# Kernel optimization log

Hardware: AMD Instinct MI355X
Metric: run time of the kernel (lower is better)

## Reference

```python
import jax, jax.numpy as jnp
import numpy as np

N = 524288
IN_C = 128
OUT_C = 128
NUM_GRAPHS = 64
NUM_STROKES = 8192
EPS = 1e-5


def setup_inputs() -> dict:
    key = jax.random.key(0)
    ks = jax.random.split(key, 8)
    x = jax.random.normal(ks[0], (N, IN_C), dtype=jnp.float32)
    batch = jnp.sort(jax.random.randint(ks[1], (N,), 0, NUM_GRAPHS))
    stroke_idx = jnp.sort(jax.random.randint(ks[2], (N,), 0, NUM_STROKES))
    s = 1.0 / np.sqrt(IN_C)
    W_max = jax.random.uniform(ks[3], (IN_C, OUT_C), jnp.float32, -s, s)
    b_max = jax.random.uniform(ks[4], (OUT_C,), jnp.float32, -s, s)
    g_max = jnp.ones((OUT_C,), jnp.float32)
    be_max = jnp.zeros((OUT_C,), jnp.float32)
    W_sk = jax.random.uniform(ks[5], (IN_C, OUT_C), jnp.float32, -s, s)
    b_sk = jax.random.uniform(ks[6], (OUT_C,), jnp.float32, -s, s)
    g_sk = jnp.ones((OUT_C,), jnp.float32)
    be_sk = jnp.zeros((OUT_C,), jnp.float32)
    return {"x": x, "batch": batch, "stroke_idx": stroke_idx,
            "W_max": W_max, "b_max": b_max, "g_max": g_max, "be_max": be_max,
            "W_sk": W_sk, "b_sk": b_sk, "g_sk": g_sk, "be_sk": be_sk}


def _mlp(x, W, b, gamma, beta):
    # Linear -> BatchNorm1d (training-mode batch stats, biased var) -> ReLU
    h = x @ W + b
    mu = jnp.mean(h, axis=0)
    var = jnp.mean((h - mu) ** 2, axis=0)
    h = (h - mu) * jax.lax.rsqrt(var + EPS) * gamma + beta
    return jax.nn.relu(h)


def reference(x, batch, stroke_idx, W_max, b_max, g_max, be_max, W_sk, b_sk, g_sk, be_sk):
    pool_max = _mlp(x, W_max, b_max, g_max, be_max)      # (N, F)
    pool_sketch = _mlp(x, W_sk, b_sk, g_sk, be_sk)       # (N, F)
    # segment max-pool per graph / per stroke, then broadcast back to nodes
    gmax = jax.ops.segment_max(pool_max, batch, num_segments=NUM_GRAPHS)       # (G, F)
    smax = jax.ops.segment_max(pool_sketch, stroke_idx, num_segments=NUM_STROKES)  # (S, F)
    pool_max = gmax[batch]          # (N, F)
    pool_sketch = smax[stroke_idx]  # (N, F)
    return jnp.concatenate([pool_sketch, pool_max], axis=1)  # (N, 2F)
```

## Files before the change

### kernel.cpp

```cpp
#include <hip/hip_runtime.h>
#include <hip/hip_bf16.h>
#include <climits>
#include <cstdint>
#include <cfloat>

#define NROWS   524288
#define KDIM    128
#define NGRAPH  64
#define NSTROKE 8192
#define EPSF    1e-5f

typedef __bf16 bf16x8 __attribute__((ext_vector_type(8)));
typedef float  f32x4  __attribute__((ext_vector_type(4)));

#define WT_OFF    0
#define CSUM_OFF  65536
#define CSQ_OFF   66560
#define ST_OFF    67584
#define GT_OFF    (ST_OFF + NSTROKE*KDIM*4)

__device__ __forceinline__ unsigned short f2bf(float f) {
  unsigned int u = __float_as_uint(f);
  u += 0x7fffu + ((u >> 16) & 1u);
  return (unsigned short)(u >> 16);
}
__device__ __forceinline__ int fkey(float f) {
  int b = __float_as_int(f);
  return b >= 0 ? b : (b ^ 0x7fffffff);
}
__device__ __forceinline__ float fdec(int k) {
  int b = k >= 0 ? k : (k ^ 0x7fffffff);
  return __int_as_float(b);
}

__global__ void k_init(const float* __restrict__ Wmax, const float* __restrict__ Wsk,
                       unsigned char* __restrict__ ws) {
  unsigned short* wt = (unsigned short*)(ws + WT_OFF);
  float* csum = (float*)(ws + CSUM_OFF);
  float* csq  = (float*)(ws + CSQ_OFF);
  int* st = (int*)(ws + ST_OFF);
  int* gt = (int*)(ws + GT_OFF);
  int i = blockIdx.x * blockDim.x + threadIdx.x;
  const int total = NSTROKE * KDIM;
  for (; i < total; i += gridDim.x * blockDim.x) {
    st[i] = INT_MIN;
    if (i < NGRAPH * KDIM) gt[i] = INT_MIN;
    if (i < 256) { csum[i] = 0.f; csq[i] = 0.f; }
    if (i < 256 * KDIM) {
      int c = i / KDIM, k = i % KDIM;
      float w = (c < 128) ? Wsk[k * 128 + c] : Wmax[k * 128 + (c - 128)];
      wt[i] = f2bf(w);
    }
  }
}

__global__ __launch_bounds__(256) void k_pass1(const float* __restrict__ x,
                                               const int* __restrict__ batch,
                                               const int* __restrict__ stroke,
                                               unsigned char* __restrict__ ws) {
  __shared__ __align__(16) unsigned short xs[2][64 * 128];
  const unsigned short* wt = (const unsigned short*)(ws + WT_OFF);
  float* csum = (float*)(ws + CSUM_OFF);
  float* csq  = (float*)(ws + CSQ_OFF);
  int* st = (int*)(ws + ST_OFF);
  int* gt = (int*)(ws + GT_OFF);

  const int tid  = threadIdx.x;
  const int lane = tid & 63;
  const int wv   = tid >> 6;
  const int lr   = lane & 15;
  const int lg   = lane >> 4;
  const int srow = tid >> 4;
  const int skg  = tid & 15;

  bf16x8 bfrag[4][4];
#pragma unroll
  for (int ks = 0; ks < 4; ++ks)
#pragma unroll
    for (int n = 0; n < 4; ++n) {
      int c = wv * 64 + n * 16 + lr;
      int k = ks * 32 + lg * 8;
      bfrag[ks][n] = *(const bf16x8*)(wt + c * KDIM + k);
    }

  float sumn[4] = {0.f, 0.f, 0.f, 0.f};
  float sqn[4]  = {0.f, 0.f, 0.f, 0.f};

  const bool isS = (wv < 2);
  const int* __restrict__ segp = isS ? stroke : batch;
  int* __restrict__ tab = isS ? st : gt;
  const int tcol = (isS ? wv : wv - 2) * 64;

  int   curseg = -1;
  float runmax[4] = {-FLT_MAX, -FLT_MAX, -FLT_MAX, -FLT_MAX};

#define FLUSH()                                                               \
  if (curseg >= 0) {                                                          \
    _Pragma("unroll")                                                         \
    for (int n = 0; n < 4; ++n) {                                             \
      float f = runmax[n];                                                    \
      f = fmaxf(f, __shfl_xor(f, 16));                                        \
      f = fmaxf(f, __shfl_xor(f, 32));                                        \
      if (lg == 0) atomicMax(&tab[curseg * KDIM + tcol + n * 16 + lr], fkey(f)); \
    }                                                                         \
  }

#define PF_LOAD(ROW0)                                                         \
  {                                                                           \
    _Pragma("unroll")                                                         \
    for (int it = 0; it < 4; ++it) {                                          \
      const float* src = x + (size_t)((ROW0) + it * 16 + srow) * KDIM + skg * 8; \
      pf[it * 2]     = *(const f32x4*)src;                                    \
      pf[it * 2 + 1] = *(const f32x4*)(src + 4);                              \
    }                                                                         \
  }

#define PF_STORE(P)                                                           \
  {                                                                           \
    _Pragma("unroll")                                                         \
    for (int it = 0; it < 4; ++it) {                                          \
      int r = it * 16 + srow;                                                 \
      union { bf16x8 v; unsigned short u[8]; } pk;                            \
      f32x4 v0 = pf[it * 2], v1 = pf[it * 2 + 1];                             \
      pk.u[0] = f2bf(v0[0]); pk.u[1] = f2bf(v0[1]);                           \
      pk.u[2] = f2bf(v0[2]); pk.u[3] = f2bf(v0[3]);                           \
      pk.u[4] = f2bf(v1[0]); pk.u[5] = f2bf(v1[1]);                           \
      pk.u[6] = f2bf(v1[2]); pk.u[7] = f2bf(v1[3]);                           \
      *(bf16x8*)(xs[P] + r * KDIM + ((skg ^ (r & 7)) << 3)) = pk.v;           \
    }                                                                         \
  }

  const int brow = blockIdx.x * 512;
  f32x4 pf[8];
  int segv, segnext;

  PF_LOAD(brow);
  segv = segp[brow + lane];
  PF_STORE(0);
  __syncthreads();

  int cur = 0;
  for (int ti = 0; ti < 8; ++ti) {
    if (ti < 7) {
      PF_LOAD(brow + (ti + 1) * 64);
      segnext = segp[brow + (ti + 1) * 64 + lane];
    }

    f32x4 acc[4][4];
#pragma unroll
    for (int m = 0; m < 4; ++m)
#pragma unroll
      for (int n = 0; n < 4; ++n) { f32x4 z = {0.f, 0.f, 0.f, 0.f}; acc[m][n] = z; }

#pragma unroll
    for (int ks = 0; ks < 4; ++ks) {
      bf16x8 af[4];
#pragma unroll
      for (int m = 0; m < 4; ++m) {
        int r  = m * 16 + lr;
        int kg = ks * 4 + lg;
        af[m] = *(const bf16x8*)(xs[cur] + r * KDIM + ((kg ^ (r & 7)) << 3));
      }
#pragma unroll
      for (int m = 0; m < 4; ++m)
#pragma unroll
        for (int n = 0; n < 4; ++n)
          acc[m][n] = __builtin_amdgcn_mfma_f32_16x16x32_bf16(af[m], bfrag[ks][n], acc[m][n], 0, 0, 0);
    }

    float tm[4];
#pragma unroll
    for (int n = 0; n < 4; ++n) {
      float s = 0.f, q = 0.f, t = -FLT_MAX;
#pragma unroll
      for (int m = 0; m < 4; ++m)
#pragma unroll
        for (int rg = 0; rg < 4; ++rg) {
          float v = acc[m][n][rg];
          s += v; q = fmaf(v, v, q); t = fmaxf(t, v);
        }
      sumn[n] += s; sqn[n] += q; tm[n] = t;
    }

    {
      int pv = __shfl_up(segv, 1);
      unsigned long long mask = __ballot(lane > 0 && pv != segv);
      if (mask == 0ull) {
        int seg0 = __shfl(segv, 0);
        if (seg0 == curseg) {
#pragma unroll
          for (int n = 0; n < 4; ++n) runmax[n] = fmaxf(runmax[n], tm[n]);
        } else {
          FLUSH();
          curseg = seg0;
#pragma unroll
          for (int n = 0; n < 4; ++n) runmax[n] = tm[n];
        }
      } else {
        unsigned long long rem = mask;
        int a = 0;
        while (true) {
          int b = rem ? (int)__builtin_ctzll(rem) : 64;
          int segr = __shfl(segv, a);
          float rm[4] = {-FLT_MAX, -FLT_MAX, -FLT_MAX, -FLT_MAX};
#pragma unroll
          for (int m = 0; m < 4; ++m)
#pragma unroll
            for (int rg = 0; rg < 4; ++rg) {
              int pos = m * 16 + lg * 4 + rg;
              bool in = (pos >= a) && (pos < b);
#pragma unroll
              for (int n = 0; n < 4; ++n)
                rm[n] = in ? fmaxf(rm[n], acc[m][n][rg]) : rm[n];
            }
          if (a == 0 && segr == curseg) {
#pragma unroll
            for (int n = 0; n < 4; ++n) runmax[n] = fmaxf(runmax[n], rm[n]);
          } else {
            FLUSH();
            curseg = segr;
#pragma unroll
            for (int n = 0; n < 4; ++n) runmax[n] = rm[n];
          }
          if (b >= 64) break;
          rem &= rem - 1; a = b;
        }
      }
    }

    if (ti < 7) {
      PF_STORE(cur ^ 1);
      segv = segnext;
    }
    __syncthreads();
    cur ^= 1;
  }

  FLUSH();

#pragma unroll
  for (int n = 0; n < 4; ++n) {
    sumn[n] += __shfl_xor(sumn[n], 16);
    sumn[n] += __shfl_xor(sumn[n], 32);
    sqn[n]  += __shfl_xor(sqn[n], 16);
    sqn[n]  += __shfl_xor(sqn[n], 32);
  }
  float s = 0.f, q = 0.f;
#pragma unroll
  for (int n = 0; n < 4; ++n) if (n == lg) { s = sumn[n]; q = sqn[n]; }
  atomicAdd(&csum[tid], s);
  atomicAdd(&csq[tid], q);
#undef FLUSH
#undef PF_LOAD
#undef PF_STORE
}

__global__ __launch_bounds__(256) void k_out(const int* __restrict__ batch,
                                             const int* __restrict__ stroke,
                                             const float* __restrict__ g_max,
                                             const float* __restrict__ be_max,
                                             const float* __restrict__ g_sk,
                                             const float* __restrict__ be_sk,
                                             const unsigned char* __restrict__ ws,
                                             float* __restrict__ out) {
  const float* csum = (const float*)(ws + CSUM_OFF);
  const float* csq  = (const float*)(ws + CSQ_OFF);
  const int* st = (const int*)(ws + ST_OFF);
  const int* gt = (const int*)(ws + GT_OFF);

  const int lane = threadIdx.x & 63;
  const int wvid = blockIdx.x * 4 + (threadIdx.x >> 6);
  const int row0 = wvid * 64;
  const bool isS = lane < 32;
  const int  cg  = (isS ? lane : lane - 32) * 4;
  const int* tab  = isS ? st : gt;
  const int* idxp = isS ? stroke : batch;
  const float* gv = isS ? g_sk : g_max;
  const float* bv = isS ? be_sk : be_max;

  const float invN = 1.0f / (float)NROWS;
  f32x4 mu, sc, bb;
#pragma unroll
  for (int j = 0; j < 4; ++j) {
    int cc = (isS ? 0 : 128) + cg + j;
    float m  = csum[cc] * invN;
    float vr = csq[cc] * invN - m * m;
    mu[j] = m;
    sc[j] = gv[cg + j] * rsqrtf(vr + EPSF);
    bb[j] = bv[cg + j];
  }

  f32x4* out4 = (f32x4*)out;
#pragma unroll 4
  for (int r = 0; r < 64; ++r) {
    int row = row0 + r;
    int seg = idxp[row];
    const int4 k4 = *(const int4*)(tab + (size_t)seg * KDIM + cg);
    f32x4 v;
    v[0] = fdec(k4.x); v[1] = fdec(k4.y); v[2] = fdec(k4.z); v[3] = fdec(k4.w);
#pragma unroll
    for (int j = 0; j < 4; ++j) v[j] = fmaxf(0.f, (v[j] - mu[j]) * sc[j] + bb[j]);
    __builtin_nontemporal_store(v, &out4[(size_t)row * 64 + lane]);
  }
}

extern "C" void kernel_launch(void* const* d_in, const int* in_sizes, int n_in,
                              void* d_out, int out_size, void* d_ws, size_t ws_size,
                              hipStream_t stream) {
  const float* x      = (const float*)d_in[0];
  const int*   batch  = (const int*)d_in[1];
  const int*   stroke = (const int*)d_in[2];
  const float* Wmax   = (const float*)d_in[3];
  const float* g_max  = (const float*)d_in[5];
  const float* be_max = (const float*)d_in[6];
  const float* Wsk    = (const float*)d_in[7];
  const float* g_sk   = (const float*)d_in[9];
  const float* be_sk  = (const float*)d_in[10];
  unsigned char* ws = (unsigned char*)d_ws;
  float* out = (float*)d_out;

  k_init <<<2048, 512, 0, stream>>>(Wmax, Wsk, ws);
  k_pass1<<<1024, 256, 0, stream>>>(x, batch, stroke, ws);
  k_out  <<<2048, 256, 0, stream>>>(batch, stroke, g_max, be_max, g_sk, be_sk, ws, out);
}
```

Measured before the change: 244.0 us.

## Split pass1 work across 8 waves with 32 output columns each

The GEMM+segment-max kernel now runs 512 threads per block, with each wave owning 32 output columns instead of 64. This halves per-thread accumulators, B fragments and prefetch registers, which should raise occupancy and hide more latency. In exchange there are more redundant A-fragment LDS reads per tile, plus more segment-boundary scans and atomics, because more waves each handle the same rows.

```diff
diff --git a/kernel.cpp b/kernel.cpp
--- a/kernel.cpp
+++ b/kernel.cpp
@@ -54,10 +54,10 @@
   }
 }
 
-__global__ __launch_bounds__(256) void k_pass1(const float* __restrict__ x,
-                                               const int* __restrict__ batch,
-                                               const int* __restrict__ stroke,
-                                               unsigned char* __restrict__ ws) {
+__global__ __launch_bounds__(512, 4) void k_pass1(const float* __restrict__ x,
+                                                  const int* __restrict__ batch,
+                                                  const int* __restrict__ stroke,
+                                                  unsigned char* __restrict__ ws) {
   __shared__ __align__(16) unsigned short xs[2][64 * 128];
   const unsigned short* wt = (const unsigned short*)(ws + WT_OFF);
   float* csum = (float*)(ws + CSUM_OFF);
@@ -70,34 +70,32 @@
   const int wv   = tid >> 6;
   const int lr   = lane & 15;
   const int lg   = lane >> 4;
-  const int srow = tid >> 4;
-  const int skg  = tid & 15;
-
-  bf16x8 bfrag[4][4];
-#pragma unroll
-  for (int ks = 0; ks < 4; ++ks)
-#pragma unroll
-    for (int n = 0; n < 4; ++n) {
-      int c = wv * 64 + n * 16 + lr;
-      int k = ks * 32 + lg * 8;
-      bfrag[ks][n] = *(const bf16x8*)(wt + c * KDIM + k);
-    }
-
-  float sumn[4] = {0.f, 0.f, 0.f, 0.f};
-  float sqn[4]  = {0.f, 0.f, 0.f, 0.f};
-
-  const bool isS = (wv < 2);
+  const int srow = tid >> 3;
+  const int skg  = tid & 7;
+
+  const int colbase = wv * 32;
+  const bool isS = (wv < 4);
   const int* __restrict__ segp = isS ? stroke : batch;
   int* __restrict__ tab = isS ? st : gt;
-  const int tcol = (isS ? wv : wv - 2) * 64;
+  const int tcol = colbase - (isS ? 0 : 128);
+
+  bf16x8 bfrag[4][2];
+#pragma unroll
+  for (int ks = 0; ks < 4; ++ks)
+#pragma unroll
+    for (int n = 0; n < 2; ++n)
+      bfrag[ks][n] = *(const bf16x8*)(wt + (colbase + n * 16 + lr) * KDIM + ks * 32 + lg * 8);
+
+  float sumn[2] = {0.f, 0.f};
+  float sqn[2]  = {0.f, 0.f};
 
   int   curseg = -1;
-  float runmax[4] = {-FLT_MAX, -FLT_MAX, -FLT_MAX, -FLT_MAX};
+  float runmax[2] = {-FLT_MAX, -FLT_MAX};
 
 #define FLUSH()                                                               \
   if (curseg >= 0) {                                                          \
     _Pragma("unroll")                                                         \
-    for (int n = 0; n < 4; ++n) {                                             \
+    for (int n = 0; n < 2; ++n) {                                             \
       float f = runmax[n];                                                    \
       f = fmaxf(f, __shfl_xor(f, 16));                                        \
       f = fmaxf(f, __shfl_xor(f, 32));                                        \
@@ -107,31 +105,30 @@
 
 #define PF_LOAD(ROW0)                                                         \
   {                                                                           \
-    _Pragma("unroll")                                                         \
-    for (int it = 0; it < 4; ++it) {                                          \
-      const float* src = x + (size_t)((ROW0) + it * 16 + srow) * KDIM + skg * 8; \
-      pf[it * 2]     = *(const f32x4*)src;                                    \
-      pf[it * 2 + 1] = *(const f32x4*)(src + 4);                              \
-    }                                                                         \
+    const float* src = x + (size_t)((ROW0) + srow) * KDIM + skg * 16;         \
+    pf[0] = *(const f32x4*)src;                                               \
+    pf[1] = *(const f32x4*)(src + 4);                                         \
+    pf[2] = *(const f32x4*)(src + 8);                                         \
+    pf[3] = *(const f32x4*)(src + 12);                                        \
   }
 
 #define PF_STORE(P)                                                           \
   {                                                                           \
-    _Pragma("unroll")                                                         \
-    for (int it = 0; it < 4; ++it) {                                          \
-      int r = it * 16 + srow;                                                 \
-      union { bf16x8 v; unsigned short u[8]; } pk;                            \
-      f32x4 v0 = pf[it * 2], v1 = pf[it * 2 + 1];                             \
-      pk.u[0] = f2bf(v0[0]); pk.u[1] = f2bf(v0[1]);                           \
-      pk.u[2] = f2bf(v0[2]); pk.u[3] = f2bf(v0[3]);                           \
-      pk.u[4] = f2bf(v1[0]); pk.u[5] = f2bf(v1[1]);                           \
-      pk.u[6] = f2bf(v1[2]); pk.u[7] = f2bf(v1[3]);                           \
-      *(bf16x8*)(xs[P] + r * KDIM + ((skg ^ (r & 7)) << 3)) = pk.v;           \
-    }                                                                         \
+    union { bf16x8 v; unsigned short u[8]; } pk;                              \
+    pk.u[0] = f2bf(pf[0][0]); pk.u[1] = f2bf(pf[0][1]);                       \
+    pk.u[2] = f2bf(pf[0][2]); pk.u[3] = f2bf(pf[0][3]);                       \
+    pk.u[4] = f2bf(pf[1][0]); pk.u[5] = f2bf(pf[1][1]);                       \
+    pk.u[6] = f2bf(pf[1][2]); pk.u[7] = f2bf(pf[1][3]);                       \
+    *(bf16x8*)(xs[P] + srow * KDIM + (((skg * 2) ^ (srow & 7)) << 3)) = pk.v; \
+    pk.u[0] = f2bf(pf[2][0]); pk.u[1] = f2bf(pf[2][1]);                       \
+    pk.u[2] = f2bf(pf[2][2]); pk.u[3] = f2bf(pf[2][3]);                       \
+    pk.u[4] = f2bf(pf[3][0]); pk.u[5] = f2bf(pf[3][1]);                       \
+    pk.u[6] = f2bf(pf[3][2]); pk.u[7] = f2bf(pf[3][3]);                       \
+    *(bf16x8*)(xs[P] + srow * KDIM + (((skg * 2 + 1) ^ (srow & 7)) << 3)) = pk.v; \
   }
 
   const int brow = blockIdx.x * 512;
-  f32x4 pf[8];
+  f32x4 pf[4];
   int segv, segnext;
 
   PF_LOAD(brow);
@@ -146,11 +143,11 @@
       segnext = segp[brow + (ti + 1) * 64 + lane];
     }
 
-    f32x4 acc[4][4];
+    f32x4 acc[4][2];
 #pragma unroll
     for (int m = 0; m < 4; ++m)
 #pragma unroll
-      for (int n = 0; n < 4; ++n) { f32x4 z = {0.f, 0.f, 0.f, 0.f}; acc[m][n] = z; }
+      for (int n = 0; n < 2; ++n) { f32x4 z = {0.f, 0.f, 0.f, 0.f}; acc[m][n] = z; }
 
 #pragma unroll
     for (int ks = 0; ks < 4; ++ks) {
@@ -162,15 +159,15 @@
         af[m] = *(const bf16x8*)(xs[cur] + r * KDIM + ((kg ^ (r & 7)) << 3));
       }
 #pragma unroll
-      for (int m = 0; m < 4; ++m)
-#pragma unroll
-        for (int n = 0; n < 4; ++n)
-          acc[m][n] = __builtin_amdgcn_mfma_f32_16x16x32_bf16(af[m], bfrag[ks][n], acc[m][n], 0, 0, 0);
-    }
-
-    float tm[4];
-#pragma unroll
-    for (int n = 0; n < 4; ++n) {
+      for (int m = 0; m < 4; ++m) {
+        acc[m][0] = __builtin_amdgcn_mfma_f32_16x16x32_bf16(af[m], bfrag[ks][0], acc[m][0], 0, 0, 0);
+        acc[m][1] = __builtin_amdgcn_mfma_f32_16x16x32_bf16(af[m], bfrag[ks][1], acc[m][1], 0, 0, 0);
+      }
+    }
+
+    float tm[2];
+#pragma unroll
+    for (int n = 0; n < 2; ++n) {
       float s = 0.f, q = 0.f, t = -FLT_MAX;
 #pragma unroll
       for (int m = 0; m < 4; ++m)
@@ -189,12 +186,12 @@
         int seg0 = __shfl(segv, 0);
         if (seg0 == curseg) {
 #pragma unroll
-          for (int n = 0; n < 4; ++n) runmax[n] = fmaxf(runmax[n], tm[n]);
+          for (int n = 0; n < 2; ++n) runmax[n] = fmaxf(runmax[n], tm[n]);
         } else {
           FLUSH();
           curseg = seg0;
 #pragma unroll
-          for (int n = 0; n < 4; ++n) runmax[n] = tm[n];
+          for (int n = 0; n < 2; ++n) runmax[n] = tm[n];
         }
       } else {
         unsigned long long rem = mask;
@@ -202,7 +199,7 @@
         while (true) {
           int b = rem ? (int)__builtin_ctzll(rem) : 64;
           int segr = __shfl(segv, a);
-          float rm[4] = {-FLT_MAX, -FLT_MAX, -FLT_MAX, -FLT_MAX};
+          float rm[2] = {-FLT_MAX, -FLT_MAX};
 #pragma unroll
           for (int m = 0; m < 4; ++m)
 #pragma unroll
@@ -210,17 +207,17 @@
               int pos = m * 16 + lg * 4 + rg;
               bool in = (pos >= a) && (pos < b);
 #pragma unroll
-              for (int n = 0; n < 4; ++n)
+              for (int n = 0; n < 2; ++n)
                 rm[n] = in ? fmaxf(rm[n], acc[m][n][rg]) : rm[n];
             }
           if (a == 0 && segr == curseg) {
 #pragma unroll
-            for (int n = 0; n < 4; ++n) runmax[n] = fmaxf(runmax[n], rm[n]);
+            for (int n = 0; n < 2; ++n) runmax[n] = fmaxf(runmax[n], rm[n]);
           } else {
             FLUSH();
             curseg = segr;
 #pragma unroll
-            for (int n = 0; n < 4; ++n) runmax[n] = rm[n];
+            for (int n = 0; n < 2; ++n) runmax[n] = rm[n];
           }
           if (b >= 64) break;
           rem &= rem - 1; a = b;
@@ -239,17 +236,15 @@
   FLUSH();
 
 #pragma unroll
-  for (int n = 0; n < 4; ++n) {
-    sumn[n] += __shfl_xor(sumn[n], 16);
-    sumn[n] += __shfl_xor(sumn[n], 32);
-    sqn[n]  += __shfl_xor(sqn[n], 16);
-    sqn[n]  += __shfl_xor(sqn[n], 32);
-  }
-  float s = 0.f, q = 0.f;
-#pragma unroll
-  for (int n = 0; n < 4; ++n) if (n == lg) { s = sumn[n]; q = sqn[n]; }
-  atomicAdd(&csum[tid], s);
-  atomicAdd(&csq[tid], q);
+  for (int n = 0; n < 2; ++n) {
+    float s = sumn[n], q = sqn[n];
+    s += __shfl_xor(s, 16); s += __shfl_xor(s, 32);
+    q += __shfl_xor(q, 16); q += __shfl_xor(q, 32);
+    if (lg == 0) {
+      atomicAdd(&csum[colbase + n * 16 + lr], s);
+      atomicAdd(&csq [colbase + n * 16 + lr], q);
+    }
+  }
 #undef FLUSH
 #undef PF_LOAD
 #undef PF_STORE
@@ -320,6 +315,6 @@
   float* out = (float*)d_out;
 
   k_init <<<2048, 512, 0, stream>>>(Wmax, Wsk, ws);
-  k_pass1<<<1024, 256, 0, stream>>>(x, batch, stroke, ws);
+  k_pass1<<<1024, 512, 0, stream>>>(x, batch, stroke, ws);
   k_out  <<<2048, 256, 0, stream>>>(batch, stroke, g_max, be_max, g_sk, be_sk, ws, out);
 }
```

Result: faster. 235.4 us, median of 2 (-3.5%).
